# Performance work log

Measured on AMD Instinct MI355X. Metric: run time of the kernel, lower is better.

## Reference

```python
import jax, jax.numpy as jnp
import numpy as np

N_NODES = 100000
N_EDGES = 1600000


def setup_inputs() -> dict:
    key = jax.random.key(0)
    ks = jax.random.split(key, 10)
    return {
        "src": jax.random.randint(ks[0], (N_EDGES,), 0, N_NODES, dtype=jnp.int32),
        "dst": jax.random.randint(ks[1], (N_EDGES,), 0, N_NODES, dtype=jnp.int32),
        "logits": jax.random.normal(ks[2], (N_NODES, 64), jnp.float32),
        "features": jax.random.normal(ks[3], (N_NODES, 512), jnp.float32),
        "proj_W": jax.random.normal(ks[4], (512, 128), jnp.float32) * 0.04,
        "proj_b": jnp.zeros((128,), jnp.float32),
        "deg_table": jax.random.normal(ks[5], (512, 64), jnp.float32) * 0.1,
        "W1": jax.random.normal(ks[6], (256, 128), jnp.float32) * 0.06,
        "b1": jnp.zeros((128,), jnp.float32),
        "W2": jax.random.normal(ks[7], (128, 64), jnp.float32) * 0.09,
        "b2": jnp.zeros((64,), jnp.float32),
    }


def _graph_conv(x, W, b, src, dst, out_deg, in_deg, n):
    # DGL GraphConv, norm='both': scale src by out_deg^-1/2, SpMM sum over
    # edges (src -> dst), scale dst by in_deg^-1/2, then bias. Weight is
    # applied before aggregation when in_feats > out_feats (true here).
    cs = jax.lax.rsqrt(jnp.maximum(out_deg, 1.0))  # [N]
    cd = jax.lax.rsqrt(jnp.maximum(in_deg, 1.0))   # [N]
    h = x * cs[:, None]
    if W.shape[0] > W.shape[1]:
        h = h @ W
        agg = jax.ops.segment_sum(h[src], dst, num_segments=n)
    else:
        agg = jax.ops.segment_sum(h[src], dst, num_segments=n) @ W
    return agg * cd[:, None] + b


def reference(src, dst, logits, features, proj_W, proj_b, deg_table, W1, b1, W2, b2):
    n = logits.shape[0]
    ones = jnp.ones(src.shape, jnp.float32)
    out_deg = jax.ops.segment_sum(ones, src, num_segments=n)  # [N]
    in_deg = jax.ops.segment_sum(ones, dst, num_segments=n)   # [N]

    feat = features @ proj_W + proj_b                          # [N, 128]
    deg_idx = (in_deg + out_deg).astype(jnp.int32)             # [N]
    deg_emb = deg_table[deg_idx]                               # [N, 64]
    x = jnp.concatenate([logits, feat, deg_emb], axis=-1)      # [N, 256]

    x = _graph_conv(x, W1, b1, src, dst, out_deg, in_deg, n)
    x = jax.nn.relu(x)  # dropout omitted (eval mode)
    x = _graph_conv(x, W2, b2, src, dst, out_deg, in_deg, n)
    return x
```

## Files before the change

### kernel.cpp

```cpp
#include <hip/hip_runtime.h>
#include <cstdint>
#include <cstddef>


typedef short short8 __attribute__((ext_vector_type(8)));
typedef float f32x4 __attribute__((ext_vector_type(4)));

__device__ __forceinline__ unsigned short f2bf(float f) {
    unsigned u = __float_as_uint(f);
    u += 0x7fff + ((u >> 16) & 1);
    return (unsigned short)(u >> 16);
}
__device__ __forceinline__ float bf2f(unsigned short s) {
    return __uint_as_float(((unsigned)s) << 16);
}

__device__ __forceinline__ void split_f4(float4 a, float4 b, short8& hv, short8& lv) {
    float f[8] = {a.x, a.y, a.z, a.w, b.x, b.y, b.z, b.w};
#pragma unroll
    for (int i = 0; i < 8; ++i) {
        unsigned u = __float_as_uint(f[i]);
        hv[i] = (short)(u >> 16);
        float r = f[i] - __uint_as_float(u & 0xffff0000u);
        lv[i] = (short)(__float_as_uint(r) >> 16);
    }
}


__global__ __launch_bounds__(256) void k_bcount(
    const int* __restrict__ src, const int* __restrict__ dst, int E,
    int* __restrict__ dcount, int* __restrict__ scount)
{
    __shared__ int dh[128], sh_[128];
    int t = threadIdx.x;
    if (t < 128) { dh[t] = 0; sh_[t] = 0; }
    __syncthreads();
    int e0 = blockIdx.x * 4096;
#pragma unroll
    for (int i = 0; i < 16; ++i) {
        int idx = e0 + t + i * 256;
        if (idx < E) {
            atomicAdd(&dh[dst[idx] >> 10], 1);
            atomicAdd(&sh_[src[idx] >> 10], 1);
        }
    }
    __syncthreads();
    if (t < 128) {
        if (dh[t]) atomicAdd(&dcount[t], dh[t]);
        if (sh_[t]) atomicAdd(&scount[t], sh_[t]);
    }
}

__global__ __launch_bounds__(128) void k_bscan(
    const int* __restrict__ dcount, const int* __restrict__ scount, int nb,
    int E, int* __restrict__ dboff, int* __restrict__ sboff,
    int* __restrict__ dcur, int* __restrict__ scur,
    int* __restrict__ rowp, int N)
{
    __shared__ int sh[128];
    int t = threadIdx.x;
    int v = (t < nb) ? dcount[t] : 0;
    sh[t] = v;
    __syncthreads();
    for (int off = 1; off < 128; off <<= 1) {
        int x = (t >= off) ? sh[t - off] : 0;
        __syncthreads();
        sh[t] += x;
        __syncthreads();
    }
    if (t < nb) { int e = sh[t] - v; dboff[t] = e; dcur[t] = e; }
    __syncthreads();
    int v2 = (t < nb) ? scount[t] : 0;
    sh[t] = v2;
    __syncthreads();
    for (int off = 1; off < 128; off <<= 1) {
        int x = (t >= off) ? sh[t - off] : 0;
        __syncthreads();
        sh[t] += x;
        __syncthreads();
    }
    if (t < nb) { int e = sh[t] - v2; sboff[t] = e; scur[t] = e; }
    if (t == 0) rowp[N] = E;
}

__global__ __launch_bounds__(256) void k_scatter2(
    const int* __restrict__ src, const int* __restrict__ dst, int E,
    int* __restrict__ dcur, int* __restrict__ scur,
    unsigned* __restrict__ ebuf, unsigned short* __restrict__ sbuf, int nb)
{
    __shared__ int dh[128], dbase[128], sh_[128], sbase[128];
    int t = threadIdx.x;
    int e0 = blockIdx.x * 4096;
    if (t < 128) { dh[t] = 0; sh_[t] = 0; }
    __syncthreads();
    int s_[16], d_[16];
#pragma unroll
    for (int i = 0; i < 16; ++i) {
        int idx = e0 + t + i * 256;
        if (idx < E) {
            s_[i] = src[idx];
            d_[i] = dst[idx];
            atomicAdd(&dh[d_[i] >> 10], 1);
            atomicAdd(&sh_[s_[i] >> 10], 1);
        } else d_[i] = -1;
    }
    __syncthreads();
    if (t < nb) {
        if (dh[t]) dbase[t] = atomicAdd(&dcur[t], dh[t]);
        if (sh_[t]) sbase[t] = atomicAdd(&scur[t], sh_[t]);
    }
    __syncthreads();
    if (t < 128) { dh[t] = 0; sh_[t] = 0; }
    __syncthreads();
#pragma unroll
    for (int i = 0; i < 16; ++i) {
        if (d_[i] >= 0) {
            int b = d_[i] >> 10;
            int p = dbase[b] + atomicAdd(&dh[b], 1);
            ebuf[p] = (unsigned)s_[i] | ((unsigned)(d_[i] & 1023) << 17);
            int bs = s_[i] >> 10;
            int q = sbase[bs] + atomicAdd(&sh_[bs], 1);
            sbuf[q] = (unsigned short)(s_[i] & 1023);
        }
    }
}

__global__ __launch_bounds__(512) void k_bucket_dst(
    const unsigned* __restrict__ ebuf, const int* __restrict__ dboff,
    const int* __restrict__ dcount, int* __restrict__ ind,
    int* __restrict__ rowp, int* __restrict__ csr, int N)
{
    __shared__ int cnt[1024];
    __shared__ int sums[512];
    int b = blockIdx.x;
    int nb0 = b << 10;
    int ncnt = min(1024, N - nb0);
    int t = threadIdx.x;
    cnt[t] = 0; cnt[t + 512] = 0;
    __syncthreads();
    int lo = dboff[b], hi = lo + dcount[b];
    for (int idx = lo + t; idx < hi; idx += 512)
        atomicAdd(&cnt[ebuf[idx] >> 17], 1);
    __syncthreads();
    int c0 = cnt[2 * t], c1 = cnt[2 * t + 1];
    sums[t] = c0 + c1;
    __syncthreads();
    for (int off = 1; off < 512; off <<= 1) {
        int x = (t >= off) ? sums[t - off] : 0;
        __syncthreads();
        sums[t] += x;
        __syncthreads();
    }
    int excl = sums[t] - (c0 + c1);
    int r0 = lo + excl, r1 = r0 + c0;
    if (2 * t < ncnt)     { rowp[nb0 + 2 * t] = r0;     ind[nb0 + 2 * t] = c0; }
    if (2 * t + 1 < ncnt) { rowp[nb0 + 2 * t + 1] = r1; ind[nb0 + 2 * t + 1] = c1; }
    __syncthreads();
    cnt[2 * t] = r0; cnt[2 * t + 1] = r1;
    __syncthreads();
    for (int idx = lo + t; idx < hi; idx += 512) {
        unsigned e = ebuf[idx];
        int p = atomicAdd(&cnt[e >> 17], 1);
        csr[p] = (int)(e & 0x1FFFF);
    }
}

__global__ __launch_bounds__(512) void k_bucket_src(
    const unsigned short* __restrict__ sbuf, const int* __restrict__ sboff,
    const int* __restrict__ scount, int* __restrict__ outd, int N)
{
    __shared__ int cnt[1024];
    int b = blockIdx.x;
    int nb0 = b << 10;
    int ncnt = min(1024, N - nb0);
    int t = threadIdx.x;
    cnt[t] = 0; cnt[t + 512] = 0;
    __syncthreads();
    int lo = sboff[b], hi = lo + scount[b];
    for (int idx = lo + t; idx < hi; idx += 512)
        atomicAdd(&cnt[sbuf[idx]], 1);
    __syncthreads();
    if (t < ncnt) outd[nb0 + t] = cnt[t];
    if (t + 512 < ncnt) outd[nb0 + t + 512] = cnt[t + 512];
}

__global__ __launch_bounds__(256) void k_norms(
    const int* __restrict__ outd, const int* __restrict__ ind, int N,
    float* __restrict__ cs, float* __restrict__ cd, int* __restrict__ didx)
{
    int i = blockIdx.x * 256 + threadIdx.x;
    if (i < N) {
        int od = outd[i], id = ind[i];
        cs[i] = rsqrtf((float)(od > 0 ? od : 1));
        cd[i] = rsqrtf((float)(id > 0 ? id : 1));
        int d = od + id;
        didx[i] = d > 511 ? 511 : d;
    }
}

__global__ __launch_bounds__(256) void k_wf(
    const float* __restrict__ projW, const float* __restrict__ W1,
    float* __restrict__ WF)
{
    int idx = blockIdx.x * 256 + threadIdx.x;
    int k = idx >> 7, j = idx & 127;
    const float* a = projW + (size_t)k * 128;
    float s = 0.f;
#pragma unroll 8
    for (int m = 0; m < 128; ++m) s = fmaf(a[m], W1[(size_t)(64 + m) * 128 + j], s);
    WF[idx] = s;
}

__global__ void k_cb(const float* __restrict__ projb, const float* __restrict__ W1,
                     float* __restrict__ cb)
{
    int j = threadIdx.x;
    float s = 0.f;
    for (int m = 0; m < 128; ++m) s = fmaf(projb[m], W1[(size_t)(64 + m) * 128 + j], s);
    cb[j] = s;
}

__global__ __launch_bounds__(256) void k_wt1(
    const float* __restrict__ WF, const float* __restrict__ W1,
    unsigned short* __restrict__ wtf_hi, unsigned short* __restrict__ wtf_lo)
{
    int idx = blockIdx.x * 256 + threadIdx.x;
    int e = idx & 7;
    int lane = (idx >> 3) & 63;
    int ci = (idx >> 9) & 7;
    int t = idx >> 12;
    int j = ci * 16 + (lane & 15);
    int k = t * 32 + (lane >> 4) * 8 + e;
    float v;
    if (k < 512) v = WF[(size_t)k * 128 + j];
    else if (k < 576) v = W1[(size_t)(k - 512) * 128 + j];
    else v = W1[(size_t)(192 + (k - 576)) * 128 + j];
    unsigned short h = f2bf(v);
    wtf_hi[idx] = h;
    float r = v - bf2f(h);
    wtf_lo[idx] = (unsigned short)(__float_as_uint(r) >> 16);
}

__global__ __launch_bounds__(256) void k_wt2(
    const float* __restrict__ W2,
    unsigned short* __restrict__ w2tf_hi, unsigned short* __restrict__ w2tf_lo)
{
    int idx = blockIdx.x * 256 + threadIdx.x;
    int e = idx & 7;
    int lane = (idx >> 3) & 63;
    int ci = (idx >> 9) & 3;
    int t = idx >> 11;
    int j = ci * 16 + (lane & 15);
    int k = t * 32 + (lane >> 4) * 8 + e;
    float v = W2[(size_t)k * 64 + j];
    unsigned short h = f2bf(v);
    w2tf_hi[idx] = h;
    float r = v - bf2f(h);
    w2tf_lo[idx] = (unsigned short)(__float_as_uint(r) >> 16);
}


#define H1_LOADA(S, t)                                                        \
    {                                                                         \
        const float* p0_ = aptr((t), r0, dd0);                                \
        A##S##0 = *(const float4*)p0_;  A##S##1 = *(const float4*)(p0_ + 4);  \
        const float* p1_ = aptr((t), r1, dd1);                                \
        A##S##2 = *(const float4*)p1_;  A##S##3 = *(const float4*)(p1_ + 4);  \
    }

#define H1_STEP(t, S)                                                         \
    {                                                                         \
        int cbuf = (t) & 1;                                                   \
        if ((t) + 1 < NT) {                                                   \
            const unsigned short* g_ = wtf_hi + (size_t)((t) + 1) * 4096 + tid * 8;  \
            sbh0 = *(const uint4*)g_;                                         \
            sbh1 = *(const uint4*)(g_ + 2048);                                \
            const unsigned short* g2_ = wtf_lo + (size_t)((t) + 1) * 4096 + tid * 8; \
            sbl0 = *(const uint4*)g2_;                                        \
            sbl1 = *(const uint4*)(g2_ + 2048);                               \
        }                                                                     \
        short8 ah0, al0, ah1, al1;                                            \
        split_f4(A##S##0, A##S##1, ah0, al0);                                 \
        split_f4(A##S##2, A##S##3, ah1, al1);                                 \
        if ((t) + 4 < NT) H1_LOADA(S, (t) + 4)                                \
        _Pragma("unroll")                                                     \
        for (int ci = 0; ci < 8; ++ci) {                                      \
            short8 bh = *(const short8*)&Bh[cbuf][ci * 512 + lane * 8];       \
            short8 bl = *(const short8*)&Bl[cbuf][ci * 512 + lane * 8];       \
            acc[0][ci] = __builtin_amdgcn_mfma_f32_16x16x32_bf16(ah0, bh, acc[0][ci], 0, 0, 0); \
            acc[0][ci] = __builtin_amdgcn_mfma_f32_16x16x32_bf16(al0, bh, acc[0][ci], 0, 0, 0); \
            acc[0][ci] = __builtin_amdgcn_mfma_f32_16x16x32_bf16(ah0, bl, acc[0][ci], 0, 0, 0); \
            acc[1][ci] = __builtin_amdgcn_mfma_f32_16x16x32_bf16(ah1, bh, acc[1][ci], 0, 0, 0); \
            acc[1][ci] = __builtin_amdgcn_mfma_f32_16x16x32_bf16(al1, bh, acc[1][ci], 0, 0, 0); \
            acc[1][ci] = __builtin_amdgcn_mfma_f32_16x16x32_bf16(ah1, bl, acc[1][ci], 0, 0, 0); \
        }                                                                     \
        if ((t) + 1 < NT) {                                                   \
            *(uint4*)&Bh[cbuf ^ 1][tid * 8] = sbh0;                           \
            *(uint4*)&Bh[cbuf ^ 1][2048 + tid * 8] = sbh1;                    \
            *(uint4*)&Bl[cbuf ^ 1][tid * 8] = sbl0;                           \
            *(uint4*)&Bl[cbuf ^ 1][2048 + tid * 8] = sbl1;                    \
        }                                                                     \
        __syncthreads();                                                      \
    }

__global__ __launch_bounds__(256, 2) void k_h1(
    const float* __restrict__ logits, const float* __restrict__ features,
    const float* __restrict__ deg_table, const int* __restrict__ didx,
    const unsigned short* __restrict__ wtf_hi, const unsigned short* __restrict__ wtf_lo,
    const float* __restrict__ cb, const float* __restrict__ cs,
    unsigned short* __restrict__ h1, int N)
{
    constexpr int NT = 20;
    __shared__ __align__(16) short Bh[2][4096];
    __shared__ __align__(16) short Bl[2][4096];
    int tid = threadIdx.x;
    int lane = tid & 63, w = tid >> 6;
    int fr = lane & 15, kg = lane >> 4;
    int i0 = blockIdx.x * 128 + w * 32;
    int r0 = i0 + fr;       if (r0 >= N) r0 = N - 1;
    int r1 = i0 + 16 + fr;  if (r1 >= N) r1 = N - 1;
    int dd0 = didx[r0], dd1 = didx[r1];

    f32x4 acc[2][8];
#pragma unroll
    for (int ri = 0; ri < 2; ++ri)
#pragma unroll
        for (int ci = 0; ci < 8; ++ci) acc[ri][ci] = (f32x4)0.f;

    auto aptr = [&](int t, int r, int dd) -> const float* {
        if (t < 16) return features  + (size_t)r * 512 + t * 32 + kg * 8;
        if (t < 18) return logits    + (size_t)r * 64 + (t - 16) * 32 + kg * 8;
        return deg_table + (size_t)dd * 64 + (t - 18) * 32 + kg * 8;
    };

    float4 A00, A01, A02, A03;
    float4 A10, A11, A12, A13;
    float4 A20, A21, A22, A23;
    float4 A30, A31, A32, A33;
    uint4 sbh0, sbh1, sbl0, sbl1;

    H1_LOADA(0, 0)
    H1_LOADA(1, 1)
    H1_LOADA(2, 2)
    H1_LOADA(3, 3)
    {
        const unsigned short* g_ = wtf_hi + tid * 8;
        sbh0 = *(const uint4*)g_;
        sbh1 = *(const uint4*)(g_ + 2048);
        const unsigned short* g2_ = wtf_lo + tid * 8;
        sbl0 = *(const uint4*)g2_;
        sbl1 = *(const uint4*)(g2_ + 2048);
        *(uint4*)&Bh[0][tid * 8] = sbh0;
        *(uint4*)&Bh[0][2048 + tid * 8] = sbh1;
        *(uint4*)&Bl[0][tid * 8] = sbl0;
        *(uint4*)&Bl[0][2048 + tid * 8] = sbl1;
    }
    __syncthreads();

    for (int tt = 0; tt < NT; tt += 4) {
        H1_STEP(tt + 0, 0)
        H1_STEP(tt + 1, 1)
        H1_STEP(tt + 2, 2)
        H1_STEP(tt + 3, 3)
    }

    float cbv[8];
#pragma unroll
    for (int ci = 0; ci < 8; ++ci) cbv[ci] = cb[ci * 16 + fr];
#pragma unroll
    for (int ri = 0; ri < 2; ++ri) {
#pragma unroll
        for (int j = 0; j < 4; ++j) {
            int row = i0 + ri * 16 + kg * 4 + j;
            if (row < N) {
                float scv = cs[row];
#pragma unroll
                for (int ci = 0; ci < 8; ++ci) {
                    h1[(size_t)row * 128 + ci * 16 + fr] =
                        f2bf(scv * (acc[ri][ci][j] + cbv[ci]));
                }
            }
        }
    }
}

__global__ __launch_bounds__(256) void k_agg1(
    const unsigned short* __restrict__ h1, const int* __restrict__ rowp,
    const int* __restrict__ csr, const float* __restrict__ cd,
    const float* __restrict__ b1, float* __restrict__ y, int N)
{
    int i = blockIdx.x * 4 + (threadIdx.x >> 6);
    if (i >= N) return;
    int lane = threadIdx.x & 63;
    int s0 = rowp[i], s1 = rowp[i + 1];
    float ax = 0.f, ay = 0.f;
    int e = s0;
    for (; e + 8 <= s1; e += 8) {
        unsigned u0 = *(const unsigned*)(h1 + (size_t)csr[e + 0] * 128 + lane * 2);
        unsigned u1 = *(const unsigned*)(h1 + (size_t)csr[e + 1] * 128 + lane * 2);
        unsigned u2 = *(const unsigned*)(h1 + (size_t)csr[e + 2] * 128 + lane * 2);
        unsigned u3 = *(const unsigned*)(h1 + (size_t)csr[e + 3] * 128 + lane * 2);
        unsigned u4 = *(const unsigned*)(h1 + (size_t)csr[e + 4] * 128 + lane * 2);
        unsigned u5 = *(const unsigned*)(h1 + (size_t)csr[e + 5] * 128 + lane * 2);
        unsigned u6 = *(const unsigned*)(h1 + (size_t)csr[e + 6] * 128 + lane * 2);
        unsigned u7 = *(const unsigned*)(h1 + (size_t)csr[e + 7] * 128 + lane * 2);
        ax += ((__uint_as_float(u0 << 16) + __uint_as_float(u1 << 16)) +
               (__uint_as_float(u2 << 16) + __uint_as_float(u3 << 16))) +
              ((__uint_as_float(u4 << 16) + __uint_as_float(u5 << 16)) +
               (__uint_as_float(u6 << 16) + __uint_as_float(u7 << 16)));
        ay += ((__uint_as_float(u0 & 0xffff0000u) + __uint_as_float(u1 & 0xffff0000u)) +
               (__uint_as_float(u2 & 0xffff0000u) + __uint_as_float(u3 & 0xffff0000u))) +
              ((__uint_as_float(u4 & 0xffff0000u) + __uint_as_float(u5 & 0xffff0000u)) +
               (__uint_as_float(u6 & 0xffff0000u) + __uint_as_float(u7 & 0xffff0000u)));
    }
    for (; e < s1; ++e) {
        unsigned u = *(const unsigned*)(h1 + (size_t)csr[e] * 128 + lane * 2);
        ax += __uint_as_float(u << 16);
        ay += __uint_as_float(u & 0xffff0000u);
    }
    float cdi = cd[i];
    float2 o;
    o.x = fmaxf(fmaf(ax, cdi, b1[lane * 2 + 0]), 0.f);
    o.y = fmaxf(fmaf(ay, cdi, b1[lane * 2 + 1]), 0.f);
    *(float2*)(y + (size_t)i * 128 + lane * 2) = o;
}

__global__ __launch_bounds__(256, 3) void k_h2(
    const float* __restrict__ y,
    const unsigned short* __restrict__ w2tf_hi, const unsigned short* __restrict__ w2tf_lo,
    const float* __restrict__ cs, unsigned short* __restrict__ h2, int N)
{
    constexpr int NT = 4;
    __shared__ __align__(16) short B2h[8192];
    __shared__ __align__(16) short B2l[8192];
    int tid = threadIdx.x;
    int lane = tid & 63, w = tid >> 6;
    int fr = lane & 15, kg = lane >> 4;
    int i0 = blockIdx.x * 128 + w * 32;
    int r0 = i0 + fr;       if (r0 >= N) r0 = N - 1;
    int r1 = i0 + 16 + fr;  if (r1 >= N) r1 = N - 1;
    const float* a0 = y + (size_t)r0 * 128 + kg * 8;
    const float* a1 = y + (size_t)r1 * 128 + kg * 8;

#pragma unroll
    for (int i = 0; i < 4; ++i) {
        *(uint4*)&B2h[(i * 256 + tid) * 8] = *(const uint4*)(w2tf_hi + (size_t)(i * 256 + tid) * 8);
        *(uint4*)&B2l[(i * 256 + tid) * 8] = *(const uint4*)(w2tf_lo + (size_t)(i * 256 + tid) * 8);
    }
    __syncthreads();

    f32x4 acc[2][4];
#pragma unroll
    for (int ri = 0; ri < 2; ++ri)
#pragma unroll
        for (int ci = 0; ci < 4; ++ci) acc[ri][ci] = (f32x4)0.f;

    float4 ar00 = *(const float4*)(a0);
    float4 ar01 = *(const float4*)(a0 + 4);
    float4 ar10 = *(const float4*)(a1);
    float4 ar11 = *(const float4*)(a1 + 4);

    for (int t = 0; t < NT; ++t) {
        short8 ah0, al0, ah1, al1;
        split_f4(ar00, ar01, ah0, al0);
        split_f4(ar10, ar11, ah1, al1);
        if (t + 1 < NT) {
            ar00 = *(const float4*)(a0 + (t + 1) * 32);
            ar01 = *(const float4*)(a0 + (t + 1) * 32 + 4);
            ar10 = *(const float4*)(a1 + (t + 1) * 32);
            ar11 = *(const float4*)(a1 + (t + 1) * 32 + 4);
        }
#pragma unroll
        for (int ci = 0; ci < 4; ++ci) {
            short8 bh = *(const short8*)&B2h[((t * 4 + ci) * 64 + lane) * 8];
            short8 bl = *(const short8*)&B2l[((t * 4 + ci) * 64 + lane) * 8];
            acc[0][ci] = __builtin_amdgcn_mfma_f32_16x16x32_bf16(ah0, bh, acc[0][ci], 0, 0, 0);
            acc[0][ci] = __builtin_amdgcn_mfma_f32_16x16x32_bf16(al0, bh, acc[0][ci], 0, 0, 0);
            acc[0][ci] = __builtin_amdgcn_mfma_f32_16x16x32_bf16(ah0, bl, acc[0][ci], 0, 0, 0);
            acc[1][ci] = __builtin_amdgcn_mfma_f32_16x16x32_bf16(ah1, bh, acc[1][ci], 0, 0, 0);
            acc[1][ci] = __builtin_amdgcn_mfma_f32_16x16x32_bf16(al1, bh, acc[1][ci], 0, 0, 0);
            acc[1][ci] = __builtin_amdgcn_mfma_f32_16x16x32_bf16(ah1, bl, acc[1][ci], 0, 0, 0);
        }
    }

#pragma unroll
    for (int ri = 0; ri < 2; ++ri) {
#pragma unroll
        for (int j = 0; j < 4; ++j) {
            int row = i0 + ri * 16 + kg * 4 + j;
            if (row < N) {
                float scv = cs[row];
#pragma unroll
                for (int ci = 0; ci < 4; ++ci) {
                    h2[(size_t)row * 64 + ci * 16 + fr] = f2bf(scv * acc[ri][ci][j]);
                }
            }
        }
    }
}

__global__ __launch_bounds__(256) void k_agg2(
    const unsigned short* __restrict__ h2, const int* __restrict__ rowp,
    const int* __restrict__ csr, const float* __restrict__ cd,
    const float* __restrict__ b2, float* __restrict__ out, int N)
{
    int i = blockIdx.x * 8 + (threadIdx.x >> 5);
    if (i >= N) return;
    int lane = threadIdx.x & 31;
    int s0 = rowp[i], s1 = rowp[i + 1];
    float ax = 0.f, ay = 0.f;
    int e = s0;
    for (; e + 8 <= s1; e += 8) {
        unsigned u0 = *(const unsigned*)(h2 + (size_t)csr[e + 0] * 64 + lane * 2);
        unsigned u1 = *(const unsigned*)(h2 + (size_t)csr[e + 1] * 64 + lane * 2);
        unsigned u2 = *(const unsigned*)(h2 + (size_t)csr[e + 2] * 64 + lane * 2);
        unsigned u3 = *(const unsigned*)(h2 + (size_t)csr[e + 3] * 64 + lane * 2);
        unsigned u4 = *(const unsigned*)(h2 + (size_t)csr[e + 4] * 64 + lane * 2);
        unsigned u5 = *(const unsigned*)(h2 + (size_t)csr[e + 5] * 64 + lane * 2);
        unsigned u6 = *(const unsigned*)(h2 + (size_t)csr[e + 6] * 64 + lane * 2);
        unsigned u7 = *(const unsigned*)(h2 + (size_t)csr[e + 7] * 64 + lane * 2);
        ax += ((__uint_as_float(u0 << 16) + __uint_as_float(u1 << 16)) +
               (__uint_as_float(u2 << 16) + __uint_as_float(u3 << 16))) +
              ((__uint_as_float(u4 << 16) + __uint_as_float(u5 << 16)) +
               (__uint_as_float(u6 << 16) + __uint_as_float(u7 << 16)));
        ay += ((__uint_as_float(u0 & 0xffff0000u) + __uint_as_float(u1 & 0xffff0000u)) +
               (__uint_as_float(u2 & 0xffff0000u) + __uint_as_float(u3 & 0xffff0000u))) +
              ((__uint_as_float(u4 & 0xffff0000u) + __uint_as_float(u5 & 0xffff0000u)) +
               (__uint_as_float(u6 & 0xffff0000u) + __uint_as_float(u7 & 0xffff0000u)));
    }
    for (; e < s1; ++e) {
        unsigned u = *(const unsigned*)(h2 + (size_t)csr[e] * 64 + lane * 2);
        ax += __uint_as_float(u << 16);
        ay += __uint_as_float(u & 0xffff0000u);
    }
    float cdi = cd[i];
    float2 o;
    o.x = fmaf(ax, cdi, b2[lane * 2 + 0]);
    o.y = fmaf(ay, cdi, b2[lane * 2 + 1]);
    *(float2*)(out + (size_t)i * 64 + lane * 2) = o;
}

extern "C" void kernel_launch(void* const* d_in, const int* in_sizes, int n_in,
                              void* d_out, int out_size, void* d_ws, size_t ws_size,
                              hipStream_t stream)
{
    const int* src = (const int*)d_in[0];
    const int* dst = (const int*)d_in[1];
    const float* logits = (const float*)d_in[2];
    const float* features = (const float*)d_in[3];
    const float* projW = (const float*)d_in[4];
    const float* projb = (const float*)d_in[5];
    const float* deg_table = (const float*)d_in[6];
    const float* W1 = (const float*)d_in[7];
    const float* b1 = (const float*)d_in[8];
    const float* W2 = (const float*)d_in[9];
    const float* b2 = (const float*)d_in[10];
    const int E = in_sizes[0];
    const int N = in_sizes[2] / 64;

    char* base = (char*)d_ws;
    size_t off = 0;
    auto alloc = [&](size_t bytes) -> void* {
        void* p = base + off;
        off += (bytes + 255) & ~(size_t)255;
        return p;
    };
    int* outd   = (int*)alloc((size_t)N * 4);
    int* ind    = (int*)alloc((size_t)N * 4);
    int* rowp   = (int*)alloc((size_t)(N + 1) * 4);
    int* csr    = (int*)alloc((size_t)E * 4);
    unsigned* ebuf = (unsigned*)alloc((size_t)E * 4);
    unsigned short* sbuf = (unsigned short*)alloc((size_t)E * 2);
    int* didx   = (int*)alloc((size_t)N * 4);
    float* cs   = (float*)alloc((size_t)N * 4);
    float* cd   = (float*)alloc((size_t)N * 4);
    float* WF   = (float*)alloc((size_t)512 * 128 * 4);
    float* cb   = (float*)alloc((size_t)128 * 4);
    int* dcount = (int*)alloc(128 * 4);
    int* scount = (int*)alloc(128 * 4);
    int* dboff  = (int*)alloc(128 * 4);
    int* sboff  = (int*)alloc(128 * 4);
    int* dcur   = (int*)alloc(128 * 4);
    int* scur   = (int*)alloc(128 * 4);
    unsigned short* wtf_hi  = (unsigned short*)alloc((size_t)81920 * 2);
    unsigned short* wtf_lo  = (unsigned short*)alloc((size_t)81920 * 2);
    unsigned short* w2tf_hi = (unsigned short*)alloc((size_t)8192 * 2);
    unsigned short* w2tf_lo = (unsigned short*)alloc((size_t)8192 * 2);
    unsigned short* h1 = (unsigned short*)alloc((size_t)N * 128 * 2);
    float* yb   = (float*)alloc((size_t)N * 128 * 4);
    unsigned short* h2 = h1;
    float* outp = (float*)d_out;

    hipMemsetAsync(dcount, 0, 128 * 4, stream);
    hipMemsetAsync(scount, 0, 128 * 4, stream);

    int nb = (N + 255) / 256;
    int mb = (N + 127) / 128;
    int ebk = (E + 4095) / 4096;
    int nbuck = (N + 1023) / 1024;

    k_bcount<<<ebk, 256, 0, stream>>>(src, dst, E, dcount, scount);
    k_bscan<<<1, 128, 0, stream>>>(dcount, scount, nbuck, E, dboff, sboff, dcur, scur, rowp, N);
    k_scatter2<<<ebk, 256, 0, stream>>>(src, dst, E, dcur, scur, ebuf, sbuf, nbuck);
    k_bucket_dst<<<nbuck, 512, 0, stream>>>(ebuf, dboff, dcount, ind, rowp, csr, N);
    k_bucket_src<<<nbuck, 512, 0, stream>>>(sbuf, sboff, scount, outd, N);
    k_norms<<<nb, 256, 0, stream>>>(outd, ind, N, cs, cd, didx);
    k_wf<<<256, 256, 0, stream>>>(projW, W1, WF);
    k_cb<<<1, 128, 0, stream>>>(projb, W1, cb);
    k_wt1<<<320, 256, 0, stream>>>(WF, W1, wtf_hi, wtf_lo);
    k_wt2<<<32, 256, 0, stream>>>(W2, w2tf_hi, w2tf_lo);
    k_h1<<<mb, 256, 0, stream>>>(logits, features, deg_table, didx, wtf_hi, wtf_lo, cb, cs, h1, N);
    k_agg1<<<(N + 3) / 4, 256, 0, stream>>>(h1, rowp, csr, cd, b1, yb, N);
    k_h2<<<mb, 256, 0, stream>>>(yb, w2tf_hi, w2tf_lo, cs, h2, N);
    k_agg2<<<(N + 7) / 8, 256, 0, stream>>>(h2, rowp, csr, cd, b2, outp, N);
}
```

Before: 333.5 us.

## Stream projection weights via direct global-to-LDS loads and shorten A prefetch depth

In the first GEMM kernel (k_h1), the hi/lo bf16 weight tiles now go straight from global memory to LDS with global_load_lds, so they no longer stage through registers and separate LDS stores. Synchronisation now uses explicit vmcnt waits and a raw s_barrier with sched_barriers, and each step issues the next tile's LDS load before computing. The A-operand prefetch depth drops from 4 tiles to 2 to free registers. The cost is a shallower look-ahead for feature loads and hand-counted vmcnt values that must match the number of outstanding loads.

```diff
diff --git a/kernel.cpp b/kernel.cpp
--- a/kernel.cpp
+++ b/kernel.cpp
@@ -24,6 +24,12 @@
         float r = f[i] - __uint_as_float(u & 0xffff0000u);
         lv[i] = (short)(__float_as_uint(r) >> 16);
     }
+}
+
+__device__ __forceinline__ void glds16(const unsigned short* g, short* l) {
+    __builtin_amdgcn_global_load_lds(
+        (const __attribute__((address_space(1))) unsigned int*)g,
+        (__attribute__((address_space(3))) unsigned int*)l, 16, 0, 0);
 }
 
 
@@ -260,33 +266,36 @@
 }
 
 
-#define H1_LOADA(S, t)                                                        \
+#define H1_STEP(t, S0, S1, S2, S3)                                            \
     {                                                                         \
-        const float* p0_ = aptr((t), r0, dd0);                                \
-        A##S##0 = *(const float4*)p0_;  A##S##1 = *(const float4*)(p0_ + 4);  \
-        const float* p1_ = aptr((t), r1, dd1);                                \
-        A##S##2 = *(const float4*)p1_;  A##S##3 = *(const float4*)(p1_ + 4);  \
-    }
-
-#define H1_STEP(t, S)                                                         \
-    {                                                                         \
-        int cbuf = (t) & 1;                                                   \
+        if ((t) == NT - 1) { asm volatile("s_waitcnt vmcnt(0)" ::: "memory"); } \
+        else               { asm volatile("s_waitcnt vmcnt(4)" ::: "memory"); } \
+        __builtin_amdgcn_sched_barrier(0);                                    \
+        __builtin_amdgcn_s_barrier();                                         \
+        __builtin_amdgcn_sched_barrier(0);                                    \
+        const int cbuf_ = (t) & 1;                                            \
         if ((t) + 1 < NT) {                                                   \
-            const unsigned short* g_ = wtf_hi + (size_t)((t) + 1) * 4096 + tid * 8;  \
-            sbh0 = *(const uint4*)g_;                                         \
-            sbh1 = *(const uint4*)(g_ + 2048);                                \
-            const unsigned short* g2_ = wtf_lo + (size_t)((t) + 1) * 4096 + tid * 8; \
-            sbl0 = *(const uint4*)g2_;                                        \
-            sbl1 = *(const uint4*)(g2_ + 2048);                               \
+            const unsigned short* gh_ = wtf_hi + (size_t)((t) + 1) * 4096 + tid * 8; \
+            const unsigned short* gl_ = wtf_lo + (size_t)((t) + 1) * 4096 + tid * 8; \
+            glds16(gh_,        &Bh[cbuf_ ^ 1][tid * 8]);                      \
+            glds16(gh_ + 2048, &Bh[cbuf_ ^ 1][2048 + tid * 8]);               \
+            glds16(gl_,        &Bl[cbuf_ ^ 1][tid * 8]);                      \
+            glds16(gl_ + 2048, &Bl[cbuf_ ^ 1][2048 + tid * 8]);               \
         }                                                                     \
+        __builtin_amdgcn_sched_barrier(0);                                    \
         short8 ah0, al0, ah1, al1;                                            \
-        split_f4(A##S##0, A##S##1, ah0, al0);                                 \
-        split_f4(A##S##2, A##S##3, ah1, al1);                                 \
-        if ((t) + 4 < NT) H1_LOADA(S, (t) + 4)                                \
+        split_f4(S0, S1, ah0, al0);                                           \
+        split_f4(S2, S3, ah1, al1);                                           \
+        if ((t) + 2 < NT) {                                                   \
+            const float* p0_ = aptr((t) + 2, r0, dd0);                        \
+            S0 = *(const float4*)p0_;  S1 = *(const float4*)(p0_ + 4);        \
+            const float* p1_ = aptr((t) + 2, r1, dd1);                        \
+            S2 = *(const float4*)p1_;  S3 = *(const float4*)(p1_ + 4);        \
+        }                                                                     \
         _Pragma("unroll")                                                     \
         for (int ci = 0; ci < 8; ++ci) {                                      \
-            short8 bh = *(const short8*)&Bh[cbuf][ci * 512 + lane * 8];       \
-            short8 bl = *(const short8*)&Bl[cbuf][ci * 512 + lane * 8];       \
+            short8 bh = *(const short8*)&Bh[cbuf_][ci * 512 + lane * 8];      \
+            short8 bl = *(const short8*)&Bl[cbuf_][ci * 512 + lane * 8];      \
             acc[0][ci] = __builtin_amdgcn_mfma_f32_16x16x32_bf16(ah0, bh, acc[0][ci], 0, 0, 0); \
             acc[0][ci] = __builtin_amdgcn_mfma_f32_16x16x32_bf16(al0, bh, acc[0][ci], 0, 0, 0); \
             acc[0][ci] = __builtin_amdgcn_mfma_f32_16x16x32_bf16(ah0, bl, acc[0][ci], 0, 0, 0); \
@@ -294,13 +303,6 @@
             acc[1][ci] = __builtin_amdgcn_mfma_f32_16x16x32_bf16(al1, bh, acc[1][ci], 0, 0, 0); \
             acc[1][ci] = __builtin_amdgcn_mfma_f32_16x16x32_bf16(ah1, bl, acc[1][ci], 0, 0, 0); \
         }                                                                     \
-        if ((t) + 1 < NT) {                                                   \
-            *(uint4*)&Bh[cbuf ^ 1][tid * 8] = sbh0;                           \
-            *(uint4*)&Bh[cbuf ^ 1][2048 + tid * 8] = sbh1;                    \
-            *(uint4*)&Bl[cbuf ^ 1][tid * 8] = sbl0;                           \
-            *(uint4*)&Bl[cbuf ^ 1][2048 + tid * 8] = sbl1;                    \
-        }                                                                     \
-        __syncthreads();                                                      \
     }
 
 __global__ __launch_bounds__(256, 2) void k_h1(
@@ -333,35 +335,28 @@
         return deg_table + (size_t)dd * 64 + (t - 18) * 32 + kg * 8;
     };
 
-    float4 A00, A01, A02, A03;
-    float4 A10, A11, A12, A13;
-    float4 A20, A21, A22, A23;
-    float4 A30, A31, A32, A33;
-    uint4 sbh0, sbh1, sbl0, sbl1;
-
-    H1_LOADA(0, 0)
-    H1_LOADA(1, 1)
-    H1_LOADA(2, 2)
-    H1_LOADA(3, 3)
+    float4 SA0, SA1, SA2, SA3;
+    float4 SB0, SB1, SB2, SB3;
+
+    glds16(wtf_hi + tid * 8,        &Bh[0][tid * 8]);
+    glds16(wtf_hi + 2048 + tid * 8, &Bh[0][2048 + tid * 8]);
+    glds16(wtf_lo + tid * 8,        &Bl[0][tid * 8]);
+    glds16(wtf_lo + 2048 + tid * 8, &Bl[0][2048 + tid * 8]);
+    __builtin_amdgcn_sched_barrier(0);
     {
-        const unsigned short* g_ = wtf_hi + tid * 8;
-        sbh0 = *(const uint4*)g_;
-        sbh1 = *(const uint4*)(g_ + 2048);
-        const unsigned short* g2_ = wtf_lo + tid * 8;
-        sbl0 = *(const uint4*)g2_;
-        sbl1 = *(const uint4*)(g2_ + 2048);
-        *(uint4*)&Bh[0][tid * 8] = sbh0;
-        *(uint4*)&Bh[0][2048 + tid * 8] = sbh1;
-        *(uint4*)&Bl[0][tid * 8] = sbl0;
-        *(uint4*)&Bl[0][2048 + tid * 8] = sbl1;
-    }
-    __syncthreads();
-
-    for (int tt = 0; tt < NT; tt += 4) {
-        H1_STEP(tt + 0, 0)
-        H1_STEP(tt + 1, 1)
-        H1_STEP(tt + 2, 2)
-        H1_STEP(tt + 3, 3)
+        const float* p0_ = aptr(0, r0, dd0);
+        SA0 = *(const float4*)p0_;  SA1 = *(const float4*)(p0_ + 4);
+        const float* p1_ = aptr(0, r1, dd1);
+        SA2 = *(const float4*)p1_;  SA3 = *(const float4*)(p1_ + 4);
+        const float* q0_ = aptr(1, r0, dd0);
+        SB0 = *(const float4*)q0_;  SB1 = *(const float4*)(q0_ + 4);
+        const float* q1_ = aptr(1, r1, dd1);
+        SB2 = *(const float4*)q1_;  SB3 = *(const float4*)(q1_ + 4);
+    }
+
+    for (int tt = 0; tt < NT; tt += 2) {
+        H1_STEP(tt + 0, SA0, SA1, SA2, SA3)
+        H1_STEP(tt + 1, SB0, SB1, SB2, SB3)
     }
 
     float cbv[8];
```

Result: no change. 333.8 us (+0.1%).
